# Kernel optimization log

Measured on AMD Instinct MI355X. Metric: run time of the kernel, lower is better.

## Reference

```python
import jax, jax.numpy as jnp
import numpy as np

B, S, H = 128, 1000, 256


def setup_inputs() -> dict:
    key = jax.random.key(0)
    ks = jax.random.split(key, 15)
    sc = 1.0 / np.sqrt(H)
    f = lambda k, shape: (jax.random.normal(k, shape, jnp.float32) * sc)
    return dict(
        static_hidden=jax.random.normal(ks[0], (B, S, H), jnp.float32),
        state_embedding=jax.random.normal(ks[1], (B, 1, H), jnp.float32),
        decoder_hidden=jax.random.normal(ks[2], (B, 1, H), jnp.float32),
        target_hidden=jax.random.normal(ks[3], (B, 1, H), jnp.float32),
        last_hh=jax.random.normal(ks[4], (1, B, H), jnp.float32),
        W_ih=f(ks[5], (3 * H, H)),
        W_hh=f(ks[6], (3 * H, H)),
        b_ih=f(ks[7], (3 * H,)),
        b_hh=f(ks[8], (3 * H,)),
        v_attn_enc=f(ks[9], (H,)),
        W_attn_enc=f(ks[10], (H, 2 * H)),
        v_attn_tgt=f(ks[11], (H,)),
        W_attn_tgt=f(ks[12], (H, 2 * H)),
        v_ptr=f(ks[13], (H,)),
        W_ptr=f(ks[14], (H, 3 * H)),
    )


def _attention(static, dec, v, W):
    # static: [B,S,H], dec: [B,1,H] -> softmax attention over S
    hid = jnp.concatenate([static, jnp.broadcast_to(dec, static.shape)], axis=2)  # [B,S,2H]
    t = jnp.tanh(jnp.einsum('hk,bsk->bhs', W, hid))  # [B,H,S]
    return jax.nn.softmax(jnp.einsum('h,bhs->bs', v, t), axis=1)  # [B,S]


def _gru_step(x, h, Wih, Whh, bih, bhh):
    # single-layer single-step torch GRU semantics; x,h: [B,H]
    gi = x @ Wih.T + bih
    gh = h @ Whh.T + bhh
    ir, iz, ig = jnp.split(gi, 3, axis=-1)
    hr, hz, hg = jnp.split(gh, 3, axis=-1)
    r = jax.nn.sigmoid(ir + hr)
    z = jax.nn.sigmoid(iz + hz)
    n = jnp.tanh(ig + r * hg)
    return (1.0 - z) * n + z * h


def _pointer_branch(static, state_emb, attn, v, W):
    context = jnp.einsum('bs,bsh->bh', attn, static)[:, None, :]  # [B,1,H]
    energy = jnp.concatenate(
        [static,
         jnp.broadcast_to(context, static.shape),
         jnp.broadcast_to(state_emb, static.shape)], axis=2)  # [B,S,3H]
    return jnp.einsum('h,bhs->bs', v, jnp.tanh(jnp.einsum('hk,bsk->bhs', W, energy)))


def reference(static_hidden, state_embedding, decoder_hidden, target_hidden, last_hh,
              W_ih, W_hh, b_ih, b_hh,
              v_attn_enc, W_attn_enc, v_attn_tgt, W_attn_tgt, v_ptr, W_ptr):
    # GRU step (dropout is identity in eval / p=0.0)
    h_new = _gru_step(decoder_hidden[:, 0, :], last_hh[0], W_ih, W_hh, b_ih, b_hh)
    rnn_out = h_new[:, None, :]  # [B,1,H]
    last_hh_new = h_new[None]    # [1,B,H]

    enc_attn = _attention(static_hidden, rnn_out, v_attn_enc, W_attn_enc)
    probs = _pointer_branch(static_hidden, state_embedding, enc_attn, v_ptr, W_ptr)

    tgt_attn = _attention(static_hidden, target_hidden, v_attn_tgt, W_attn_tgt)
    # NOTE: original code reuses self.v / self.W (not v_target/W_taret) for the
    # target branch energy -- replicated faithfully.
    probs_target = _pointer_branch(static_hidden, state_embedding, tgt_attn, v_ptr, W_ptr)

    return (5.0 * probs + probs_target, last_hh_new)
```

## Files before the change

kernel.cpp:

```cpp
#include <hip/hip_runtime.h>
#include <hip/hip_bf16.h>
#include <stdint.h>
#include <stddef.h>

#define Bn 128
#define Sn 1000
#define SP 1024
#define Hn 256

typedef __bf16 bf16;
typedef __bf16 bf16x8 __attribute__((ext_vector_type(8)));
typedef __bf16 bf16x4 __attribute__((ext_vector_type(4)));
typedef float  f32x4  __attribute__((ext_vector_type(4)));

typedef __attribute__((address_space(1))) const unsigned int* gas1;
typedef __attribute__((address_space(3))) unsigned int* las3;

__device__ __forceinline__ float fast_tanh(float x){
  return 1.0f - 2.0f / (__expf(2.0f * x) + 1.0f);
}
__device__ __forceinline__ float fast_sigmoid(float x){
  return 1.0f / (1.0f + __expf(-x));
}
__device__ __forceinline__ float dot4(float4 a, float4 b){
  return a.x*b.x + a.y*b.y + a.z*b.z + a.w*b.w;
}
__device__ __forceinline__ float wave_reduce(float v){
  #pragma unroll
  for (int o=1;o<64;o<<=1) v += __shfl_xor(v, o);
  return v;
}

__global__ void k0a_convert(const float* __restrict__ stat, bf16* __restrict__ Abf){
  int p = blockIdx.x * 256 + threadIdx.x;
  int row = p >> 5;
  int ch  = p & 31;
  int s = row & (SP - 1);
  int b = row >> 10;
  float4 f0 = make_float4(0.f,0.f,0.f,0.f), f1 = f0;
  if (s < Sn){
    const float4* src = (const float4*)(stat + ((size_t)(b*Sn + s))*Hn + ch*8);
    f0 = src[0]; f1 = src[1];
  }
  bf16x8 v;
  v[0]=(bf16)f0.x; v[1]=(bf16)f0.y; v[2]=(bf16)f0.z; v[3]=(bf16)f0.w;
  v[4]=(bf16)f1.x; v[5]=(bf16)f1.y; v[6]=(bf16)f1.z; v[7]=(bf16)f1.w;
  *(bf16x8*)(Abf + (size_t)row*Hn + ch*8) = v;
}

__global__ void k0b_weights(const float* __restrict__ We, const float* __restrict__ Wt,
                            const float* __restrict__ Wp, bf16* __restrict__ Wcb){
  int t = blockIdx.x * 256 + threadIdx.x;
  int r = t >> 8, c = t & 255;
  float val;
  if (r < 256)       val = We[r*512 + c];
  else if (r < 512)  val = Wt[(r-256)*512 + c];
  else               val = Wp[(r-512)*768 + c];
  Wcb[t] = (bf16)val;
}

__global__ __launch_bounds__(1024) void k1_gru(
    const float* __restrict__ dec, const float* __restrict__ lhh,
    const float* __restrict__ tgt, const float* __restrict__ se,
    const float* __restrict__ Wih, const float* __restrict__ Whh,
    const float* __restrict__ bih, const float* __restrict__ bhh,
    const float* __restrict__ We,  const float* __restrict__ Wt,
    const float* __restrict__ Wp,
    float* __restrict__ out_hh, float* __restrict__ d_enc,
    float* __restrict__ d_tgt,  float* __restrict__ c3){
  __shared__ __align__(16) float xs[256], hs[256], ts[256], ss[256], hn[256];
  __shared__ float gi[768], gh[768];
  int b = blockIdx.x, t = threadIdx.x;
  int wid = t >> 6, ln = t & 63;
  if (t < 256){
    xs[t] = dec[b*256 + t]; hs[t] = lhh[b*256 + t];
    ts[t] = tgt[b*256 + t]; ss[t] = se[b*256 + t];
  }
  __syncthreads();
  #pragma unroll 2
  for (int k = 0; k < 96; k++){
    int vr = k*16 + wid;
    const float* wr; const float* xv;
    int r;
    if (vr < 768){ r = vr;      wr = Wih + (size_t)r*256; xv = xs; }
    else         { r = vr-768;  wr = Whh + (size_t)r*256; xv = hs; }
    float d = dot4(((const float4*)wr)[ln], ((const float4*)xv)[ln]);
    d = wave_reduce(d);
    if (ln == 0){
      if (vr < 768) gi[r] = d + bih[r];
      else          gh[r] = d + bhh[r];
    }
  }
  __syncthreads();
  if (t < 256){
    float r = fast_sigmoid(gi[t] + gh[t]);
    float z = fast_sigmoid(gi[256+t] + gh[256+t]);
    float n = fast_tanh(gi[512+t] + r*gh[512+t]);
    float h = (1.f - z)*n + z*hs[t];
    hn[t] = h;
    out_hh[b*256 + t] = h;
  }
  __syncthreads();
  #pragma unroll 2
  for (int k = 0; k < 48; k++){
    int vr = k*16 + wid;
    const float* wr; const float* xv; float* dst; int r;
    if (vr < 256)      { r = vr;     wr = We + (size_t)r*512 + 256; xv = hn; dst = d_enc; }
    else if (vr < 512) { r = vr-256; wr = Wt + (size_t)r*512 + 256; xv = ts; dst = d_tgt; }
    else               { r = vr-512; wr = Wp + (size_t)r*768 + 512; xv = ss; dst = c3; }
    float d = dot4(((const float4*)wr)[ln], ((const float4*)xv)[ln]);
    d = wave_reduce(d);
    if (ln == 0) dst[b*256 + r] = d;
  }
}

__global__ __launch_bounds__(512) void k2_gemm(
    const bf16* __restrict__ Abf, const bf16* __restrict__ Wcb,
    const float* __restrict__ d_enc, const float* __restrict__ d_tgt,
    const float* __restrict__ v_enc, const float* __restrict__ v_tgt,
    float* __restrict__ sc_e, float* __restrict__ sc_t, bf16* __restrict__ Aptr){
  __shared__ __align__(16) bf16 As[64*256];
  __shared__ __align__(16) bf16 Bs[2][128*64];
  __shared__ float pS[2][64];
  int tid = threadIdx.x, w = tid>>6, l = tid&63;
  int st = blockIdx.x, b = blockIdx.y;
  int wm = (w&3)*16, wn = (w>>2)*64;
  int lm = l&15, q = l>>4;
  if (tid < 64){ pS[0][tid]=0.f; pS[1][tid]=0.f; }

  {
    const bf16* gA = Abf + ((size_t)(b*SP + st*64))*Hn;
    int rl = w*2 + (l>>5);
    int ch = l & 31;
    #pragma unroll
    for (int is=0; is<4; is++){
      int row = is*16 + rl;
      int sc_ = ch ^ (row & 7);
      __builtin_amdgcn_global_load_lds((gas1)(gA + (size_t)row*256 + sc_*8),
                                       (las3)(&As[(is*16 + w*2)*256]), 16, 0, 0);
    }
  }

  for (int p=0; p<3; p++){
    f32x4 acc[2][4];
    #pragma unroll
    for (int u=0;u<2;u++)
      #pragma unroll
      for (int j=0;j<4;j++) acc[u][j] = (f32x4){0.f,0.f,0.f,0.f};

    for (int kt=0; kt<4; kt++){
      __syncthreads();
      #pragma unroll
      for (int buf=0; buf<2; buf++){
        int nc = p*2 + buf;
        #pragma unroll
        for (int is=0; is<2; is++){
          int row = w*16 + is*8 + (l>>3);
          int sc_ = (l&7) ^ (row & 7);
          __builtin_amdgcn_global_load_lds(
              (gas1)(Wcb + ((size_t)(nc*128 + row))*256 + kt*64 + sc_*8),
              (las3)(&Bs[buf][(w*16 + is*8)*64]), 16, 0, 0);
        }
      }
      __syncthreads();
      #pragma unroll
      for (int kk=0; kk<2; kk++){
        bf16x8 af;
        {
          int rA = wm + lm;
          int c = (kt*8 + kk*4 + q) ^ (rA & 7);
          af = *(const bf16x8*)(&As[rA*256 + c*8]);
        }
        #pragma unroll
        for (int buf=0; buf<2; buf++){
          #pragma unroll
          for (int j=0;j<4;j++){
            int rB = wn + j*16 + lm;
            int cB = (kk*4 + q) ^ (rB & 7);
            bf16x8 bf_ = *(const bf16x8*)(&Bs[buf][rB*64 + cB*8]);
            acc[buf][j] = __builtin_amdgcn_mfma_f32_16x16x32_bf16(af, bf_, acc[buf][j], 0,0,0);
          }
        }
      }
    }

    if (p < 2){
      const float* vv = p ? v_tgt : v_enc;
      const float* db = (p ? d_tgt : d_enc) + b*256;
      #pragma unroll
      for (int buf=0; buf<2; buf++){
        float vj[4], dj[4];
        #pragma unroll
        for (int j=0;j<4;j++){
          int hh = buf*128 + wn + j*16 + lm;
          vj[j] = vv[hh]; dj[j] = db[hh];
        }
        #pragma unroll
        for (int r=0;r<4;r++){
          float pp = 0.f;
          #pragma unroll
          for (int j=0;j<4;j++) pp += vj[j]*fast_tanh(acc[buf][j][r] + dj[j]);
          pp += __shfl_xor(pp,1); pp += __shfl_xor(pp,2);
          pp += __shfl_xor(pp,4); pp += __shfl_xor(pp,8);
          if (lm == 0) atomicAdd(&pS[p][wm + q*4 + r], pp);
        }
      }
    } else {
      bf16* dst = Aptr + ((size_t)(b*16 + st))*16384;
      #pragma unroll
      for (int buf=0; buf<2; buf++){
        #pragma unroll
        for (int r=0;r<4;r++){
          bf16x4 v4;
          #pragma unroll
          for (int j=0;j<4;j++) v4[j] = (bf16)acc[buf][j][r];
          int slot = buf*4 + r;
          *(bf16x4*)(dst + ((size_t)(slot*512 + tid))*4) = v4;
        }
      }
    }
  }
  __syncthreads();
  if (tid < 64)        sc_e[b*SP + st*64 + tid]        = pS[0][tid];
  else if (tid < 128)  sc_t[b*SP + st*64 + (tid-64)]   = pS[1][tid-64];
}

__global__ __launch_bounds__(256) void k3_ctx(
    const float* __restrict__ sc_e, const float* __restrict__ sc_t,
    const bf16* __restrict__ Abf, bf16* __restrict__ ctxP){
  __shared__ float attE[256], attT[256];
  __shared__ float red[16];
  int b = blockIdx.x, sq = blockIdx.y, t = threadIdx.x;
  int wid = t>>6, ln = t&63;

  float mE=-1e30f, mT=-1e30f;
  #pragma unroll
  for (int i=0;i<4;i++){
    int s = t + i*256;
    if (s < Sn){
      mE = fmaxf(mE, sc_e[b*SP+s]);
      mT = fmaxf(mT, sc_t[b*SP+s]);
    }
  }
  #pragma unroll
  for (int o=1;o<64;o<<=1){ mE=fmaxf(mE,__shfl_xor(mE,o)); mT=fmaxf(mT,__shfl_xor(mT,o)); }
  if (ln==0){ red[wid*2]=mE; red[wid*2+1]=mT; }
  __syncthreads();
  float ME = fmaxf(fmaxf(red[0],red[2]), fmaxf(red[4],red[6]));
  float MT = fmaxf(fmaxf(red[1],red[3]), fmaxf(red[5],red[7]));
  float sE=0.f, sT=0.f;
  #pragma unroll
  for (int i=0;i<4;i++){
    int s = t + i*256;
    if (s < Sn){
      sE += __expf(sc_e[b*SP+s] - ME);
      sT += __expf(sc_t[b*SP+s] - MT);
    }
  }
  #pragma unroll
  for (int o=1;o<64;o<<=1){ sE+=__shfl_xor(sE,o); sT+=__shfl_xor(sT,o); }
  __syncthreads();
  if (ln==0){ red[wid*2]=sE; red[wid*2+1]=sT; }
  __syncthreads();
  float invE = 1.f/(red[0]+red[2]+red[4]+red[6]);
  float invT = 1.f/(red[1]+red[3]+red[5]+red[7]);

  int r0 = sq*250;
  if (t < 250){
    int s = r0 + t;
    attE[t] = __expf(sc_e[b*SP+s] - ME)*invE;
    attT[t] = __expf(sc_t[b*SP+s] - MT)*invT;
  }
  __syncthreads();

  const bf16* base = Abf + ((size_t)(b*SP + r0))*Hn + t;
  float aE=0.f, aT=0.f;
  #pragma unroll 2
  for (int i=0;i<250;i++){
    float a = (float)base[(size_t)i*Hn];
    aE += attE[i]*a;
    aT += attT[i]*a;
  }
  ctxP[(((size_t)sq)*128 + b)*256 + t]       = (bf16)aE;
  ctxP[(((size_t)(4 + sq))*128 + b)*256 + t] = (bf16)aT;
}

__global__ __launch_bounds__(1024) void k3c_c2(
    const bf16* __restrict__ ctxP, const float* __restrict__ Wp,
    const float* __restrict__ c3,
    float* __restrict__ cE, float* __restrict__ cT){
  __shared__ __align__(16) float ctx[2][256];
  int b = blockIdx.x, t = threadIdx.x;
  int wid = t>>6, ln = t&63;
  if (t < 512){
    int var = t>>8, h = t&255;
    float s = 0.f;
    #pragma unroll
    for (int sqq=0; sqq<4; sqq++)
      s += (float)ctxP[(((size_t)(var*4 + sqq))*128 + b)*256 + h];
    ctx[var][h] = s;
  }
  __syncthreads();
  #pragma unroll 2
  for (int k=0;k<32;k++){
    int vr = k*16 + wid;
    int var = vr>>8, h = vr&255;
    float d = dot4(((const float4*)(Wp + (size_t)h*768 + 256))[ln],
                   ((const float4*)ctx[var])[ln]);
    d = wave_reduce(d);
    if (ln==0) (var ? cT : cE)[b*256 + h] = d + c3[b*256 + h];
  }
}

__global__ __launch_bounds__(512) void k4_final(
    const bf16* __restrict__ Aptr, const float* __restrict__ cE,
    const float* __restrict__ cT, const float* __restrict__ vp,
    float* __restrict__ out){
  __shared__ float pE[64], pT[64];
  int tid=threadIdx.x, w=tid>>6, l=tid&63;
  int st=blockIdx.x, b=blockIdx.y;
  int wm=(w&3)*16, wn=(w>>2)*64, lm=l&15, q=l>>4;
  if (tid < 64){ pE[tid]=0.f; pT[tid]=0.f; }
  __syncthreads();
  const bf16* src = Aptr + ((size_t)(b*16 + st))*16384;
  float vj[8], ej[8], tj[8];
  #pragma unroll
  for (int u=0;u<8;u++){
    int hh = (u>>2)*128 + wn + (u&3)*16 + lm;
    vj[u]=vp[hh]; ej[u]=cE[b*256+hh]; tj[u]=cT[b*256+hh];
  }
  float peR[4]={0.f,0.f,0.f,0.f}, ptR[4]={0.f,0.f,0.f,0.f};
  #pragma unroll
  for (int buf=0;buf<2;buf++){
    #pragma unroll
    for (int r=0;r<4;r++){
      bf16x4 v4 = *(const bf16x4*)(src + ((size_t)((buf*4+r)*512 + tid))*4);
      #pragma unroll
      for (int j=0;j<4;j++){
        float a = (float)v4[j];
        int u = buf*4 + j;
        peR[r] += vj[u]*fast_tanh(a + ej[u]);
        ptR[r] += vj[u]*fast_tanh(a + tj[u]);
      }
    }
  }
  #pragma unroll
  for (int r=0;r<4;r++){
    float pe = peR[r], pt = ptR[r];
    pe += __shfl_xor(pe,1); pt += __shfl_xor(pt,1);
    pe += __shfl_xor(pe,2); pt += __shfl_xor(pt,2);
    pe += __shfl_xor(pe,4); pt += __shfl_xor(pt,4);
    pe += __shfl_xor(pe,8); pt += __shfl_xor(pt,8);
    if (lm==0){
      atomicAdd(&pE[wm + q*4 + r], pe);
      atomicAdd(&pT[wm + q*4 + r], pt);
    }
  }
  __syncthreads();
  if (tid < 64){
    int s = st*64 + tid;
    if (s < Sn) out[b*Sn + s] = 5.0f*pE[tid] + pT[tid];
  }
}

extern "C" void kernel_launch(void* const* d_in, const int* in_sizes, int n_in,
                              void* d_out, int out_size, void* d_ws, size_t ws_size,
                              hipStream_t stream){
  const float* stat = (const float*)d_in[0];
  const float* se   = (const float*)d_in[1];
  const float* dec  = (const float*)d_in[2];
  const float* tgt  = (const float*)d_in[3];
  const float* lhh  = (const float*)d_in[4];
  const float* Wih  = (const float*)d_in[5];
  const float* Whh  = (const float*)d_in[6];
  const float* bih  = (const float*)d_in[7];
  const float* bhh  = (const float*)d_in[8];
  const float* vEnc = (const float*)d_in[9];
  const float* WEnc = (const float*)d_in[10];
  const float* vTgt = (const float*)d_in[11];
  const float* WTgt = (const float*)d_in[12];
  const float* vPtr = (const float*)d_in[13];
  const float* WPtr = (const float*)d_in[14];
  float* out = (float*)d_out;

  char* wsp = (char*)d_ws;
  bf16*  Abf  = (bf16*)(wsp);
  bf16*  Aptr = (bf16*)(wsp + 67108864);
  bf16*  Wcb  = (bf16*)(wsp + 134217728);
  float* dEnc = (float*)(wsp + 134610944);
  bf16*  ctxP = (bf16*)(wsp + 134217728);
  float* dTgt = (float*)(wsp + 134742016);
  float* scE  = (float*)(wsp + 134873088);
  float* scT  = (float*)(wsp + 135397376);
  float* c3   = (float*)(wsp + 135921664);
  float* cE   = (float*)(wsp + 136052736);
  float* cT   = (float*)(wsp + 136183808);

  hipLaunchKernelGGL(k0a_convert, dim3(16384), dim3(256), 0, stream, stat, Abf);
  hipLaunchKernelGGL(k0b_weights, dim3(768), dim3(256), 0, stream, WEnc, WTgt, WPtr, Wcb);
  hipLaunchKernelGGL(k1_gru, dim3(128), dim3(1024), 0, stream,
                     dec, lhh, tgt, se, Wih, Whh, bih, bhh, WEnc, WTgt, WPtr,
                     out + Bn*Sn, dEnc, dTgt, c3);
  hipLaunchKernelGGL(k2_gemm, dim3(16, 128), dim3(512), 0, stream,
                     Abf, Wcb, dEnc, dTgt, vEnc, vTgt, scE, scT, Aptr);
  hipLaunchKernelGGL(k3_ctx, dim3(128, 4), dim3(256), 0, stream,
                     scE, scT, Abf, ctxP);
  hipLaunchKernelGGL(k3c_c2, dim3(128), dim3(1024), 0, stream,
                     ctxP, WPtr, c3, cE, cT);
  hipLaunchKernelGGL(k4_final, dim3(16, 128), dim3(512), 0, stream,
                     Aptr, cE, cT, vPtr, out);
}
```

Baseline: 518.9 us.

## Fuse static fp32-to-bf16 conversion into GEMM and restructure small matvec kernels

Removes the separate pass that converted the full static tensor to bf16. The GEMM now loads fp32 static directly and converts it into swizzled shared memory, and the context kernel reads fp32 static, which drops a large write-plus-read of intermediate data. The GEMM block becomes 256 threads, each wave owning a 64-wide N slice with a 4x4 MFMA tile, which improves register reuse. The GRU and projection matvecs are rewritten as batch-parallel kernels over transposed inputs with coalesced weight-row reads. In exchange, the GEMM loses its async global-to-LDS load for A and reads twice as many bytes of fp32 input.

```diff
diff --git a/kernel.cpp b/kernel.cpp
--- a/kernel.cpp
+++ b/kernel.cpp
@@ -22,338 +22,332 @@
 __device__ __forceinline__ float fast_sigmoid(float x){
   return 1.0f / (1.0f + __expf(-x));
 }
-__device__ __forceinline__ float dot4(float4 a, float4 b){
-  return a.x*b.x + a.y*b.y + a.z*b.z + a.w*b.w;
-}
-__device__ __forceinline__ float wave_reduce(float v){
-  #pragma unroll
-  for (int o=1;o<64;o<<=1) v += __shfl_xor(v, o);
-  return v;
-}
-
-__global__ void k0a_convert(const float* __restrict__ stat, bf16* __restrict__ Abf){
-  int p = blockIdx.x * 256 + threadIdx.x;
-  int row = p >> 5;
-  int ch  = p & 31;
-  int s = row & (SP - 1);
-  int b = row >> 10;
-  float4 f0 = make_float4(0.f,0.f,0.f,0.f), f1 = f0;
-  if (s < Sn){
-    const float4* src = (const float4*)(stat + ((size_t)(b*Sn + s))*Hn + ch*8);
-    f0 = src[0]; f1 = src[1];
-  }
-  bf16x8 v;
-  v[0]=(bf16)f0.x; v[1]=(bf16)f0.y; v[2]=(bf16)f0.z; v[3]=(bf16)f0.w;
-  v[4]=(bf16)f1.x; v[5]=(bf16)f1.y; v[6]=(bf16)f1.z; v[7]=(bf16)f1.w;
-  *(bf16x8*)(Abf + (size_t)row*Hn + ch*8) = v;
-}
-
-__global__ void k0b_weights(const float* __restrict__ We, const float* __restrict__ Wt,
-                            const float* __restrict__ Wp, bf16* __restrict__ Wcb){
-  int t = blockIdx.x * 256 + threadIdx.x;
-  int r = t >> 8, c = t & 255;
-  float val;
-  if (r < 256)       val = We[r*512 + c];
-  else if (r < 512)  val = Wt[(r-256)*512 + c];
-  else               val = Wp[(r-512)*768 + c];
-  Wcb[t] = (bf16)val;
-}
-
-__global__ __launch_bounds__(1024) void k1_gru(
-    const float* __restrict__ dec, const float* __restrict__ lhh,
-    const float* __restrict__ tgt, const float* __restrict__ se,
+
+__global__ void k0w(const float* __restrict__ We, const float* __restrict__ Wt,
+                    const float* __restrict__ Wp, bf16* __restrict__ Wcb,
+                    const float* __restrict__ dec, const float* __restrict__ lhh,
+                    const float* __restrict__ tgt, const float* __restrict__ se,
+                    float* __restrict__ xT, float* __restrict__ hT,
+                    float* __restrict__ tT, float* __restrict__ sT){
+  int blk = blockIdx.x, t = threadIdx.x;
+  if (blk < 768){
+    int tt = blk*256 + t;
+    int r = tt >> 8, c = tt & 255;
+    float val;
+    if (r < 256)       val = We[r*512 + c];
+    else if (r < 512)  val = Wt[(r-256)*512 + c];
+    else               val = Wp[(r-512)*768 + c];
+    Wcb[tt] = (bf16)val;
+  } else {
+    int idx = blk - 768;
+    int a = idx >> 7, bb = idx & 127;
+    const float* src = (a==0) ? dec : (a==1) ? lhh : (a==2) ? tgt : se;
+    float* dst       = (a==0) ? xT  : (a==1) ? hT  : (a==2) ? tT  : sT;
+    dst[t*128 + bb] = src[bb*256 + t];
+  }
+}
+
+__global__ __launch_bounds__(512) void k1a_gru(
+    const float* __restrict__ xT, const float* __restrict__ hT,
     const float* __restrict__ Wih, const float* __restrict__ Whh,
     const float* __restrict__ bih, const float* __restrict__ bhh,
-    const float* __restrict__ We,  const float* __restrict__ Wt,
+    float* __restrict__ out_hh, float* __restrict__ hnT){
+  int t = threadIdx.x;
+  int g = t >> 7, b = t & 127;
+  int h = blockIdx.x*4 + g;
+  const float4* wir = (const float4*)(Wih + (size_t)h*256);
+  const float4* wiz = (const float4*)(Wih + (size_t)(256+h)*256);
+  const float4* wig = (const float4*)(Wih + (size_t)(512+h)*256);
+  const float4* whr = (const float4*)(Whh + (size_t)h*256);
+  const float4* whz = (const float4*)(Whh + (size_t)(256+h)*256);
+  const float4* whg = (const float4*)(Whh + (size_t)(512+h)*256);
+  float air=0.f, aiz=0.f, aig=0.f, ahr=0.f, ahz=0.f, ahg=0.f;
+  #pragma unroll 2
+  for (int kq=0; kq<64; kq++){
+    float4 vir = wir[kq], viz = wiz[kq], vig = wig[kq];
+    float4 vhr = whr[kq], vhz = whz[kq], vhg = whg[kq];
+    #pragma unroll
+    for (int e=0;e<4;e++){
+      int k = kq*4 + e;
+      float xv = xT[k*128 + b];
+      float hv = hT[k*128 + b];
+      float wi_r = (&vir.x)[e], wi_z = (&viz.x)[e], wi_g = (&vig.x)[e];
+      float wh_r = (&vhr.x)[e], wh_z = (&vhz.x)[e], wh_g = (&vhg.x)[e];
+      air += wi_r*xv; aiz += wi_z*xv; aig += wi_g*xv;
+      ahr += wh_r*hv; ahz += wh_z*hv; ahg += wh_g*hv;
+    }
+  }
+  air += bih[h];      ahr += bhh[h];
+  aiz += bih[256+h];  ahz += bhh[256+h];
+  aig += bih[512+h];  ahg += bhh[512+h];
+  float r = fast_sigmoid(air + ahr);
+  float z = fast_sigmoid(aiz + ahz);
+  float n = fast_tanh(aig + r*ahg);
+  float hprev = hT[h*128 + b];
+  float hnew = (1.f - z)*n + z*hprev;
+  out_hh[b*256 + h] = hnew;
+  hnT[h*128 + b] = hnew;
+}
+
+__global__ __launch_bounds__(512) void k1c_dots(
+    const float* __restrict__ hnT, const float* __restrict__ tT,
+    const float* __restrict__ sT,
+    const float* __restrict__ We, const float* __restrict__ Wt,
     const float* __restrict__ Wp,
-    float* __restrict__ out_hh, float* __restrict__ d_enc,
-    float* __restrict__ d_tgt,  float* __restrict__ c3){
-  __shared__ __align__(16) float xs[256], hs[256], ts[256], ss[256], hn[256];
-  __shared__ float gi[768], gh[768];
-  int b = blockIdx.x, t = threadIdx.x;
-  int wid = t >> 6, ln = t & 63;
-  if (t < 256){
-    xs[t] = dec[b*256 + t]; hs[t] = lhh[b*256 + t];
-    ts[t] = tgt[b*256 + t]; ss[t] = se[b*256 + t];
-  }
-  __syncthreads();
+    float* __restrict__ dEnc, float* __restrict__ dTgt, float* __restrict__ c3){
+  int t = threadIdx.x;
+  int g = t >> 7, b = t & 127;
+  int vr = blockIdx.x*4 + g;
+  int var = vr >> 8, h = vr & 255;
+  const float* wrow; const float* X; float* dst;
+  if (var == 0)      { wrow = We + (size_t)h*512 + 256; X = hnT; dst = dEnc; }
+  else if (var == 1) { wrow = Wt + (size_t)h*512 + 256; X = tT;  dst = dTgt; }
+  else               { wrow = Wp + (size_t)h*768 + 512; X = sT;  dst = c3; }
+  const float4* w4 = (const float4*)wrow;
+  float acc = 0.f;
   #pragma unroll 2
-  for (int k = 0; k < 96; k++){
-    int vr = k*16 + wid;
-    const float* wr; const float* xv;
-    int r;
-    if (vr < 768){ r = vr;      wr = Wih + (size_t)r*256; xv = xs; }
-    else         { r = vr-768;  wr = Whh + (size_t)r*256; xv = hs; }
-    float d = dot4(((const float4*)wr)[ln], ((const float4*)xv)[ln]);
-    d = wave_reduce(d);
-    if (ln == 0){
-      if (vr < 768) gi[r] = d + bih[r];
-      else          gh[r] = d + bhh[r];
-    }
-  }
-  __syncthreads();
-  if (t < 256){
-    float r = fast_sigmoid(gi[t] + gh[t]);
-    float z = fast_sigmoid(gi[256+t] + gh[256+t]);
-    float n = fast_tanh(gi[512+t] + r*gh[512+t]);
-    float h = (1.f - z)*n + z*hs[t];
-    hn[t] = h;
-    out_hh[b*256 + t] = h;
-  }
-  __syncthreads();
-  #pragma unroll 2
-  for (int k = 0; k < 48; k++){
-    int vr = k*16 + wid;
-    const float* wr; const float* xv; float* dst; int r;
-    if (vr < 256)      { r = vr;     wr = We + (size_t)r*512 + 256; xv = hn; dst = d_enc; }
-    else if (vr < 512) { r = vr-256; wr = Wt + (size_t)r*512 + 256; xv = ts; dst = d_tgt; }
-    else               { r = vr-512; wr = Wp + (size_t)r*768 + 512; xv = ss; dst = c3; }
-    float d = dot4(((const float4*)wr)[ln], ((const float4*)xv)[ln]);
-    d = wave_reduce(d);
-    if (ln == 0) dst[b*256 + r] = d;
-  }
-}
-
-__global__ __launch_bounds__(512) void k2_gemm(
-    const bf16* __restrict__ Abf, const bf16* __restrict__ Wcb,
-    const float* __restrict__ d_enc, const float* __restrict__ d_tgt,
-    const float* __restrict__ v_enc, const float* __restrict__ v_tgt,
-    float* __restrict__ sc_e, float* __restrict__ sc_t, bf16* __restrict__ Aptr){
+  for (int kq=0; kq<64; kq++){
+    float4 wv = w4[kq];
+    #pragma unroll
+    for (int e=0;e<4;e++)
+      acc += (&wv.x)[e] * X[(kq*4+e)*128 + b];
+  }
+  dst[b*256 + h] = acc;
+}
+
+__global__ __launch_bounds__(256) void k2_gemm(
+    const float* __restrict__ stat, const bf16* __restrict__ Wcb,
+    const float* __restrict__ dEnc, const float* __restrict__ dTgt,
+    const float* __restrict__ vEnc, const float* __restrict__ vTgt,
+    float* __restrict__ scE, float* __restrict__ scT, bf16* __restrict__ Aptr){
   __shared__ __align__(16) bf16 As[64*256];
-  __shared__ __align__(16) bf16 Bs[2][128*64];
+  __shared__ __align__(16) bf16 Bs[256*64];
   __shared__ float pS[2][64];
   int tid = threadIdx.x, w = tid>>6, l = tid&63;
   int st = blockIdx.x, b = blockIdx.y;
-  int wm = (w&3)*16, wn = (w>>2)*64;
   int lm = l&15, q = l>>4;
-  if (tid < 64){ pS[0][tid]=0.f; pS[1][tid]=0.f; }
+  if (tid < 128) pS[tid>>6][tid&63] = 0.f;
 
   {
-    const bf16* gA = Abf + ((size_t)(b*SP + st*64))*Hn;
-    int rl = w*2 + (l>>5);
-    int ch = l & 31;
-    #pragma unroll
-    for (int is=0; is<4; is++){
-      int row = is*16 + rl;
-      int sc_ = ch ^ (row & 7);
-      __builtin_amdgcn_global_load_lds((gas1)(gA + (size_t)row*256 + sc_*8),
-                                       (las3)(&As[(is*16 + w*2)*256]), 16, 0, 0);
+    #pragma unroll
+    for (int is=0; is<16; is++){
+      int fidx = is*256 + tid;
+      int row = fidx >> 6;
+      int col4 = fidx & 63;
+      int s = st*64 + row;
+      float4 f = make_float4(0.f,0.f,0.f,0.f);
+      if (s < Sn)
+        f = ((const float4*)(stat + ((size_t)(b*Sn + s))*Hn))[col4];
+      bf16x4 v;
+      v[0]=(bf16)f.x; v[1]=(bf16)f.y; v[2]=(bf16)f.z; v[3]=(bf16)f.w;
+      int c8 = col4 >> 1, half = col4 & 1;
+      *(bf16x4*)(&As[row*256 + ((c8 ^ (row&7))<<3) + half*4]) = v;
     }
   }
 
   for (int p=0; p<3; p++){
-    f32x4 acc[2][4];
-    #pragma unroll
-    for (int u=0;u<2;u++)
-      #pragma unroll
-      for (int j=0;j<4;j++) acc[u][j] = (f32x4){0.f,0.f,0.f,0.f};
+    f32x4 acc[4][4];
+    #pragma unroll
+    for (int i=0;i<4;i++)
+      #pragma unroll
+      for (int j=0;j<4;j++) acc[i][j] = (f32x4){0.f,0.f,0.f,0.f};
 
     for (int kt=0; kt<4; kt++){
       __syncthreads();
       #pragma unroll
-      for (int buf=0; buf<2; buf++){
-        int nc = p*2 + buf;
+      for (int is=0; is<8; is++){
+        int row = w*64 + is*8 + (l>>3);
+        int sc_ = (l&7) ^ (row & 7);
+        __builtin_amdgcn_global_load_lds(
+            (gas1)(Wcb + ((size_t)(p*256 + row))*256 + kt*64 + sc_*8),
+            (las3)(&Bs[(w*64 + is*8)*64]), 16, 0, 0);
+      }
+      __syncthreads();
+      #pragma unroll
+      for (int kk=0; kk<2; kk++){
+        bf16x8 af[4], bfr[4];
         #pragma unroll
-        for (int is=0; is<2; is++){
-          int row = w*16 + is*8 + (l>>3);
-          int sc_ = (l&7) ^ (row & 7);
-          __builtin_amdgcn_global_load_lds(
-              (gas1)(Wcb + ((size_t)(nc*128 + row))*256 + kt*64 + sc_*8),
-              (las3)(&Bs[buf][(w*16 + is*8)*64]), 16, 0, 0);
-        }
-      }
-      __syncthreads();
-      #pragma unroll
-      for (int kk=0; kk<2; kk++){
-        bf16x8 af;
-        {
-          int rA = wm + lm;
+        for (int i=0;i<4;i++){
+          int rA = i*16 + lm;
           int c = (kt*8 + kk*4 + q) ^ (rA & 7);
-          af = *(const bf16x8*)(&As[rA*256 + c*8]);
+          af[i] = *(const bf16x8*)(&As[rA*256 + c*8]);
         }
         #pragma unroll
-        for (int buf=0; buf<2; buf++){
+        for (int j=0;j<4;j++){
+          int rB = w*64 + j*16 + lm;
+          int cB = (kk*4 + q) ^ (rB & 7);
+          bfr[j] = *(const bf16x8*)(&Bs[rB*64 + cB*8]);
+        }
+        #pragma unroll
+        for (int i=0;i<4;i++)
           #pragma unroll
-          for (int j=0;j<4;j++){
-            int rB = wn + j*16 + lm;
-            int cB = (kk*4 + q) ^ (rB & 7);
-            bf16x8 bf_ = *(const bf16x8*)(&Bs[buf][rB*64 + cB*8]);
-            acc[buf][j] = __builtin_amdgcn_mfma_f32_16x16x32_bf16(af, bf_, acc[buf][j], 0,0,0);
-          }
-        }
+          for (int j=0;j<4;j++)
+            acc[i][j] = __builtin_amdgcn_mfma_f32_16x16x32_bf16(af[i], bfr[j], acc[i][j], 0,0,0);
       }
     }
 
     if (p < 2){
-      const float* vv = p ? v_tgt : v_enc;
-      const float* db = (p ? d_tgt : d_enc) + b*256;
-      #pragma unroll
-      for (int buf=0; buf<2; buf++){
-        float vj[4], dj[4];
-        #pragma unroll
-        for (int j=0;j<4;j++){
-          int hh = buf*128 + wn + j*16 + lm;
-          vj[j] = vv[hh]; dj[j] = db[hh];
-        }
+      const float* vv = p ? vTgt : vEnc;
+      const float* db = (p ? dTgt : dEnc) + b*256;
+      float vj[4], dj[4];
+      #pragma unroll
+      for (int j=0;j<4;j++){
+        int hh = w*64 + j*16 + lm;
+        vj[j] = vv[hh]; dj[j] = db[hh];
+      }
+      #pragma unroll
+      for (int i=0;i<4;i++){
         #pragma unroll
         for (int r=0;r<4;r++){
           float pp = 0.f;
           #pragma unroll
-          for (int j=0;j<4;j++) pp += vj[j]*fast_tanh(acc[buf][j][r] + dj[j]);
+          for (int j=0;j<4;j++) pp += vj[j]*fast_tanh(acc[i][j][r] + dj[j]);
           pp += __shfl_xor(pp,1); pp += __shfl_xor(pp,2);
           pp += __shfl_xor(pp,4); pp += __shfl_xor(pp,8);
-          if (lm == 0) atomicAdd(&pS[p][wm + q*4 + r], pp);
+          if (lm == 0) atomicAdd(&pS[p][i*16 + q*4 + r], pp);
         }
       }
     } else {
       bf16* dst = Aptr + ((size_t)(b*16 + st))*16384;
       #pragma unroll
-      for (int buf=0; buf<2; buf++){
+      for (int i=0;i<4;i++){
         #pragma unroll
         for (int r=0;r<4;r++){
           bf16x4 v4;
           #pragma unroll
-          for (int j=0;j<4;j++) v4[j] = (bf16)acc[buf][j][r];
-          int slot = buf*4 + r;
-          *(bf16x4*)(dst + ((size_t)(slot*512 + tid))*4) = v4;
+          for (int j=0;j<4;j++) v4[j] = (bf16)acc[i][j][r];
+          int slot = i*4 + r;
+          *(bf16x4*)(dst + ((size_t)((slot*4 + w)*64 + l))*4) = v4;
         }
       }
     }
   }
   __syncthreads();
-  if (tid < 64)        sc_e[b*SP + st*64 + tid]        = pS[0][tid];
-  else if (tid < 128)  sc_t[b*SP + st*64 + (tid-64)]   = pS[1][tid-64];
-}
-
-__global__ __launch_bounds__(256) void k3_ctx(
-    const float* __restrict__ sc_e, const float* __restrict__ sc_t,
-    const bf16* __restrict__ Abf, bf16* __restrict__ ctxP){
-  __shared__ float attE[256], attT[256];
-  __shared__ float red[16];
+  if (tid < 64)        scE[b*SP + st*64 + tid]      = pS[0][tid];
+  else if (tid < 128)  scT[b*SP + st*64 + tid-64]   = pS[1][tid-64];
+}
+
+__global__ __launch_bounds__(1024) void k3_ctx(
+    const float* __restrict__ scE, const float* __restrict__ scT,
+    const float* __restrict__ stat, float* __restrict__ ctxP){
+  __shared__ float attE[500], attT[500];
+  __shared__ float redE[16], redT[16];
+  __shared__ float pe[4][256], pt[4][256];
   int b = blockIdx.x, sq = blockIdx.y, t = threadIdx.x;
   int wid = t>>6, ln = t&63;
 
-  float mE=-1e30f, mT=-1e30f;
-  #pragma unroll
-  for (int i=0;i<4;i++){
-    int s = t + i*256;
-    if (s < Sn){
-      mE = fmaxf(mE, sc_e[b*SP+s]);
-      mT = fmaxf(mT, sc_t[b*SP+s]);
-    }
-  }
+  float vE = (t < Sn) ? scE[b*SP + t] : -1e30f;
+  float vT = (t < Sn) ? scT[b*SP + t] : -1e30f;
+  float mE = vE, mT = vT;
   #pragma unroll
   for (int o=1;o<64;o<<=1){ mE=fmaxf(mE,__shfl_xor(mE,o)); mT=fmaxf(mT,__shfl_xor(mT,o)); }
-  if (ln==0){ red[wid*2]=mE; red[wid*2+1]=mT; }
-  __syncthreads();
-  float ME = fmaxf(fmaxf(red[0],red[2]), fmaxf(red[4],red[6]));
-  float MT = fmaxf(fmaxf(red[1],red[3]), fmaxf(red[5],red[7]));
-  float sE=0.f, sT=0.f;
-  #pragma unroll
-  for (int i=0;i<4;i++){
-    int s = t + i*256;
-    if (s < Sn){
-      sE += __expf(sc_e[b*SP+s] - ME);
-      sT += __expf(sc_t[b*SP+s] - MT);
-    }
-  }
+  if (ln==0){ redE[wid]=mE; redT[wid]=mT; }
+  __syncthreads();
+  float ME=-1e30f, MT=-1e30f;
+  #pragma unroll
+  for (int i=0;i<16;i++){ ME=fmaxf(ME,redE[i]); MT=fmaxf(MT,redT[i]); }
+  __syncthreads();
+  float eE = (t < Sn) ? __expf(vE-ME) : 0.f;
+  float eT = (t < Sn) ? __expf(vT-MT) : 0.f;
+  float sE=eE, sT=eT;
   #pragma unroll
   for (int o=1;o<64;o<<=1){ sE+=__shfl_xor(sE,o); sT+=__shfl_xor(sT,o); }
-  __syncthreads();
-  if (ln==0){ red[wid*2]=sE; red[wid*2+1]=sT; }
-  __syncthreads();
-  float invE = 1.f/(red[0]+red[2]+red[4]+red[6]);
-  float invT = 1.f/(red[1]+red[3]+red[5]+red[7]);
-
-  int r0 = sq*250;
-  if (t < 250){
-    int s = r0 + t;
-    attE[t] = __expf(sc_e[b*SP+s] - ME)*invE;
-    attT[t] = __expf(sc_t[b*SP+s] - MT)*invT;
-  }
-  __syncthreads();
-
-  const bf16* base = Abf + ((size_t)(b*SP + r0))*Hn + t;
+  if (ln==0){ redE[wid]=sE; redT[wid]=sT; }
+  __syncthreads();
+  float SE=0.f, ST=0.f;
+  #pragma unroll
+  for (int i=0;i<16;i++){ SE+=redE[i]; ST+=redT[i]; }
+  float invE = 1.f/SE, invT = 1.f/ST;
+  if (t < 500){
+    int s = sq*500 + t;
+    attE[t] = __expf(scE[b*SP+s]-ME)*invE;
+    attT[t] = __expf(scT[b*SP+s]-MT)*invT;
+  }
+  __syncthreads();
+
+  int sg = t>>8, h = t&255;
+  const float* base = stat + ((size_t)(b*Sn + sq*500 + sg*125))*Hn + h;
   float aE=0.f, aT=0.f;
-  #pragma unroll 2
-  for (int i=0;i<250;i++){
-    float a = (float)base[(size_t)i*Hn];
-    aE += attE[i]*a;
-    aT += attT[i]*a;
-  }
-  ctxP[(((size_t)sq)*128 + b)*256 + t]       = (bf16)aE;
-  ctxP[(((size_t)(4 + sq))*128 + b)*256 + t] = (bf16)aT;
-}
-
-__global__ __launch_bounds__(1024) void k3c_c2(
-    const bf16* __restrict__ ctxP, const float* __restrict__ Wp,
+  #pragma unroll 4
+  for (int i=0;i<125;i++){
+    float a = base[(size_t)i*Hn];
+    aE += attE[sg*125+i]*a;
+    aT += attT[sg*125+i]*a;
+  }
+  pe[sg][h]=aE; pt[sg][h]=aT;
+  __syncthreads();
+  if (t < 256){
+    float s0 = pe[0][t]+pe[1][t]+pe[2][t]+pe[3][t];
+    ctxP[(((size_t)sq)*256 + t)*128 + b] = s0;
+  } else if (t < 512){
+    int h2 = t-256;
+    float s1 = pt[0][h2]+pt[1][h2]+pt[2][h2]+pt[3][h2];
+    ctxP[(((size_t)(2+sq))*256 + h2)*128 + b] = s1;
+  }
+}
+
+__global__ __launch_bounds__(512) void k3c_c2(
+    const float* __restrict__ ctxP, const float* __restrict__ Wp,
     const float* __restrict__ c3,
     float* __restrict__ cE, float* __restrict__ cT){
-  __shared__ __align__(16) float ctx[2][256];
-  int b = blockIdx.x, t = threadIdx.x;
-  int wid = t>>6, ln = t&63;
-  if (t < 512){
-    int var = t>>8, h = t&255;
-    float s = 0.f;
-    #pragma unroll
-    for (int sqq=0; sqq<4; sqq++)
-      s += (float)ctxP[(((size_t)(var*4 + sqq))*128 + b)*256 + h];
-    ctx[var][h] = s;
-  }
-  __syncthreads();
+  int t = threadIdx.x;
+  int g = t >> 7, b = t & 127;
+  int vr = blockIdx.x*4 + g;
+  int var = vr >> 8, h = vr & 255;
+  const float4* w4 = (const float4*)(Wp + (size_t)h*768 + 256);
+  const float* x0 = ctxP + ((size_t)(var*2))*256*128;
+  const float* x1 = ctxP + ((size_t)(var*2+1))*256*128;
+  float acc = 0.f;
   #pragma unroll 2
-  for (int k=0;k<32;k++){
-    int vr = k*16 + wid;
-    int var = vr>>8, h = vr&255;
-    float d = dot4(((const float4*)(Wp + (size_t)h*768 + 256))[ln],
-                   ((const float4*)ctx[var])[ln]);
-    d = wave_reduce(d);
-    if (ln==0) (var ? cT : cE)[b*256 + h] = d + c3[b*256 + h];
-  }
-}
-
-__global__ __launch_bounds__(512) void k4_final(
+  for (int kq=0; kq<64; kq++){
+    float4 wv = w4[kq];
+    #pragma unroll
+    for (int e=0;e<4;e++){
+      int k = kq*4+e;
+      acc += (&wv.x)[e] * (x0[k*128+b] + x1[k*128+b]);
+    }
+  }
+  (var ? cT : cE)[b*256 + h] = acc + c3[b*256 + h];
+}
+
+__global__ __launch_bounds__(256) void k4_final(
     const bf16* __restrict__ Aptr, const float* __restrict__ cE,
     const float* __restrict__ cT, const float* __restrict__ vp,
     float* __restrict__ out){
   __shared__ float pE[64], pT[64];
   int tid=threadIdx.x, w=tid>>6, l=tid&63;
   int st=blockIdx.x, b=blockIdx.y;
-  int wm=(w&3)*16, wn=(w>>2)*64, lm=l&15, q=l>>4;
+  int lm=l&15, q=l>>4;
   if (tid < 64){ pE[tid]=0.f; pT[tid]=0.f; }
   __syncthreads();
   const bf16* src = Aptr + ((size_t)(b*16 + st))*16384;
-  float vj[8], ej[8], tj[8];
-  #pragma unroll
-  for (int u=0;u<8;u++){
-    int hh = (u>>2)*128 + wn + (u&3)*16 + lm;
-    vj[u]=vp[hh]; ej[u]=cE[b*256+hh]; tj[u]=cT[b*256+hh];
-  }
-  float peR[4]={0.f,0.f,0.f,0.f}, ptR[4]={0.f,0.f,0.f,0.f};
-  #pragma unroll
-  for (int buf=0;buf<2;buf++){
+  float vj[4], ej[4], tj[4];
+  #pragma unroll
+  for (int j=0;j<4;j++){
+    int hh = w*64 + j*16 + lm;
+    vj[j]=vp[hh]; ej[j]=cE[b*256+hh]; tj[j]=cT[b*256+hh];
+  }
+  #pragma unroll
+  for (int i=0;i<4;i++){
     #pragma unroll
     for (int r=0;r<4;r++){
-      bf16x4 v4 = *(const bf16x4*)(src + ((size_t)((buf*4+r)*512 + tid))*4);
+      int slot = i*4 + r;
+      bf16x4 v4 = *(const bf16x4*)(src + ((size_t)((slot*4 + w)*64 + l))*4);
+      float pe=0.f, pt=0.f;
       #pragma unroll
       for (int j=0;j<4;j++){
         float a = (float)v4[j];
-        int u = buf*4 + j;
-        peR[r] += vj[u]*fast_tanh(a + ej[u]);
-        ptR[r] += vj[u]*fast_tanh(a + tj[u]);
-      }
-    }
-  }
-  #pragma unroll
-  for (int r=0;r<4;r++){
-    float pe = peR[r], pt = ptR[r];
-    pe += __shfl_xor(pe,1); pt += __shfl_xor(pt,1);
-    pe += __shfl_xor(pe,2); pt += __shfl_xor(pt,2);
-    pe += __shfl_xor(pe,4); pt += __shfl_xor(pt,4);
-    pe += __shfl_xor(pe,8); pt += __shfl_xor(pt,8);
-    if (lm==0){
-      atomicAdd(&pE[wm + q*4 + r], pe);
-      atomicAdd(&pT[wm + q*4 + r], pt);
+        pe += vj[j]*fast_tanh(a + ej[j]);
+        pt += vj[j]*fast_tanh(a + tj[j]);
+      }
+      pe += __shfl_xor(pe,1); pt += __shfl_xor(pt,1);
+      pe += __shfl_xor(pe,2); pt += __shfl_xor(pt,2);
+      pe += __shfl_xor(pe,4); pt += __shfl_xor(pt,4);
+      pe += __shfl_xor(pe,8); pt += __shfl_xor(pt,8);
+      if (lm==0){
+        atomicAdd(&pE[i*16 + q*4 + r], pe);
+        atomicAdd(&pT[i*16 + q*4 + r], pt);
+      }
     }
   }
   __syncthreads();
@@ -384,29 +378,34 @@
   float* out = (float*)d_out;
 
   char* wsp = (char*)d_ws;
-  bf16*  Abf  = (bf16*)(wsp);
-  bf16*  Aptr = (bf16*)(wsp + 67108864);
-  bf16*  Wcb  = (bf16*)(wsp + 134217728);
-  float* dEnc = (float*)(wsp + 134610944);
-  bf16*  ctxP = (bf16*)(wsp + 134217728);
-  float* dTgt = (float*)(wsp + 134742016);
-  float* scE  = (float*)(wsp + 134873088);
-  float* scT  = (float*)(wsp + 135397376);
-  float* c3   = (float*)(wsp + 135921664);
-  float* cE   = (float*)(wsp + 136052736);
-  float* cT   = (float*)(wsp + 136183808);
-
-  hipLaunchKernelGGL(k0a_convert, dim3(16384), dim3(256), 0, stream, stat, Abf);
-  hipLaunchKernelGGL(k0b_weights, dim3(768), dim3(256), 0, stream, WEnc, WTgt, WPtr, Wcb);
-  hipLaunchKernelGGL(k1_gru, dim3(128), dim3(1024), 0, stream,
-                     dec, lhh, tgt, se, Wih, Whh, bih, bhh, WEnc, WTgt, WPtr,
-                     out + Bn*Sn, dEnc, dTgt, c3);
-  hipLaunchKernelGGL(k2_gemm, dim3(16, 128), dim3(512), 0, stream,
-                     Abf, Wcb, dEnc, dTgt, vEnc, vTgt, scE, scT, Aptr);
-  hipLaunchKernelGGL(k3_ctx, dim3(128, 4), dim3(256), 0, stream,
-                     scE, scT, Abf, ctxP);
-  hipLaunchKernelGGL(k3c_c2, dim3(128), dim3(1024), 0, stream,
+  bf16*  Aptr = (bf16*)(wsp);
+  bf16*  Wcb  = (bf16*)(wsp + 67108864);
+  float* xT   = (float*)(wsp + 67502080);
+  float* hT   = (float*)(wsp + 67633152);
+  float* tT   = (float*)(wsp + 67764224);
+  float* sT   = (float*)(wsp + 67895296);
+  float* hnT  = (float*)(wsp + 68026368);
+  float* scE  = (float*)(wsp + 68157440);
+  float* scT  = (float*)(wsp + 68681728);
+  float* dEnc = (float*)(wsp + 69206016);
+  float* dTgt = (float*)(wsp + 69337088);
+  float* c3   = (float*)(wsp + 69468160);
+  float* cE   = (float*)(wsp + 69599232);
+  float* cT   = (float*)(wsp + 69730304);
+  float* ctxP = (float*)(wsp + 69861376);
+
+  hipLaunchKernelGGL(k0w, dim3(1280), dim3(256), 0, stream,
+                     WEnc, WTgt, WPtr, Wcb, dec, lhh, tgt, se, xT, hT, tT, sT);
+  hipLaunchKernelGGL(k1a_gru, dim3(64), dim3(512), 0, stream,
+                     xT, hT, Wih, Whh, bih, bhh, out + Bn*Sn, hnT);
+  hipLaunchKernelGGL(k1c_dots, dim3(192), dim3(512), 0, stream,
+                     hnT, tT, sT, WEnc, WTgt, WPtr, dEnc, dTgt, c3);
+  hipLaunchKernelGGL(k2_gemm, dim3(16, 128), dim3(256), 0, stream,
+                     stat, Wcb, dEnc, dTgt, vEnc, vTgt, scE, scT, Aptr);
+  hipLaunchKernelGGL(k3_ctx, dim3(128, 2), dim3(1024), 0, stream,
+                     scE, scT, stat, ctxP);
+  hipLaunchKernelGGL(k3c_c2, dim3(128), dim3(512), 0, stream,
                      ctxP, WPtr, c3, cE, cT);
-  hipLaunchKernelGGL(k4_final, dim3(16, 128), dim3(512), 0, stream,
+  hipLaunchKernelGGL(k4_final, dim3(16, 128), dim3(256), 0, stream,
                      Aptr, cE, cT, vPtr, out);
 }
```

After: 458.4 us. 1.13x faster.
